# Kernel tuning notes

Hardware: AMD Instinct MI355X
Metric: run time of the kernel (lower is better)

Reference implementation:

```python
import jax, jax.numpy as jnp
import numpy as np

EPS = 1e-5
EMBED_DIM = 1024
CTX_DIM = 768
NUM_HEADS = 16
DH = EMBED_DIM // NUM_HEADS
# Faithful to torch source: embed_dim // num_heads ** 0.5 parses as embed_dim // (num_heads**0.5)
SCALE = EMBED_DIM // (NUM_HEADS ** 0.5)  # = 256.0


def ws_conv1x1(x, w, b, mask):
    # weight-standardized 1x1 conv1d: w [O, I, 1], x [B, I, T]
    w2 = w[..., 0]
    mu = jnp.mean(w2, axis=1, keepdims=True)
    var = jnp.var(w2, axis=1, keepdims=True)
    wn = (w2 - mu) * jax.lax.rsqrt(var + EPS)
    y = jnp.einsum('oi,bit->bot', wn, x) + b[None, :, None]
    if mask is not None:
        y = jnp.where(mask, y, 0.0)  # mask [B,1,T] bool
    return y


def layernorm(x, g, b):
    # normalize over last axis
    mu = jnp.mean(x, axis=-1, keepdims=True)
    var = jnp.var(x, axis=-1, keepdims=True)
    return (x - mu) * jax.lax.rsqrt(var + EPS) * g + b


def setup_inputs() -> dict:
    key = jax.random.key(0)
    ks = jax.random.split(key, 16)
    B, T, S = 4, 1024, 1024
    inp = {
        'x': jax.random.normal(ks[0], (B, EMBED_DIM, T), dtype=jnp.float32),
        'context': jax.random.normal(ks[1], (B, CTX_DIM, S), dtype=jnp.float32),
        'mask': jax.random.randint(ks[2], (B, 1, T), 0, 2).astype(bool),
        'mask_ctx': jax.random.randint(ks[3], (B, 1, S), 0, 2).astype(bool),
        'qw': jax.random.normal(ks[4], (EMBED_DIM, EMBED_DIM, 1), dtype=jnp.float32) * 0.02,
        'qb': jnp.zeros((EMBED_DIM,), jnp.float32),
        'kw': jax.random.normal(ks[5], (EMBED_DIM, CTX_DIM, 1), dtype=jnp.float32) * 0.02,
        'kb': jnp.zeros((EMBED_DIM,), jnp.float32),
        'vw': jax.random.normal(ks[6], (EMBED_DIM, CTX_DIM, 1), dtype=jnp.float32) * 0.02,
        'vb': jnp.zeros((EMBED_DIM,), jnp.float32),
        'ow': jax.random.normal(ks[7], (EMBED_DIM, EMBED_DIM, 1), dtype=jnp.float32) * 0.02,
        'ob': jnp.zeros((EMBED_DIM,), jnp.float32),
        'gq': jnp.ones((DH,), jnp.float32), 'bq': jnp.zeros((DH,), jnp.float32),
        'gk': jnp.ones((DH,), jnp.float32), 'bk': jnp.zeros((DH,), jnp.float32),
        'gv': jnp.ones((DH,), jnp.float32), 'bv': jnp.zeros((DH,), jnp.float32),
    }
    return inp


def reference(x, context, mask, mask_ctx, qw, qb, kw, kb, vw, vb, ow, ob, gq, bq, gk, bk, gv, bv):
    B, E, T = x.shape
    S = context.shape[-1]
    q = ws_conv1x1(x, qw, qb, mask)            # [B,E,T]
    k = ws_conv1x1(context, kw, kb, mask_ctx)  # [B,E,S]
    v = ws_conv1x1(context, vw, vb, mask_ctx)  # [B,E,S]
    # split heads -> [B,H,dh,L]
    q = q.reshape(B, NUM_HEADS, DH, T)
    k = k.reshape(B, NUM_HEADS, DH, S)
    v = v.reshape(B, NUM_HEADS, DH, S)
    # middle_norm: LayerNorm over dh (applied on transposed layout)
    q = jnp.swapaxes(layernorm(jnp.swapaxes(q, -1, -2), gq, bq), -1, -2)
    k = jnp.swapaxes(layernorm(jnp.swapaxes(k, -1, -2), gk, bk), -1, -2)
    v = jnp.swapaxes(layernorm(jnp.swapaxes(v, -1, -2), gv, bv), -1, -2)
    # scores: k^T @ q -> [B,H,S,T]
    scores = jnp.einsum('bhds,bhdt->bhst', k, q) / SCALE
    scores = jnp.where(mask[:, :, None, :], scores, -1e9)  # mask over query dim T
    scores = jax.nn.softmax(scores, axis=-1)               # softmax over T (as in source)
    scores = jnp.where(mask_ctx[:, :, :, None], scores, 0.0)
    out = jnp.einsum('bhds,bhst->bhdt', v, scores)          # v @ scores -> [B,H,dh,T]
    out = out.reshape(B, E, T)
    out = ws_conv1x1(out, ow, ob, mask) + x
    return out
```

## Files before the change

kernel.cpp:

```cpp
#include <hip/hip_runtime.h>

#define NB 4
#define TT 1024
#define SS 1024
#define EE 1024
#define CCH 768
#define NH 16
#define DHH 64
#define EPSF 1e-5f
#define QSCALE (1.4426950408889634f / 256.0f)

typedef unsigned short u16;
typedef __attribute__((ext_vector_type(8))) short short8;
typedef __attribute__((ext_vector_type(8))) unsigned short u16x8;
typedef __attribute__((ext_vector_type(4))) unsigned short u16x4;
typedef __attribute__((ext_vector_type(4))) float f32x4;

__device__ __forceinline__ u16 f2bu(float f) {
    union { float f; unsigned u; } x; x.f = f;
    unsigned r = x.u + 0x7fffu + ((x.u >> 16) & 1u);
    return (u16)(r >> 16);
}
__device__ __forceinline__ float bu2f(u16 u) {
    union { unsigned u; float f; } x; x.u = ((unsigned)u) << 16; return x.f;
}

#if __has_builtin(__builtin_amdgcn_exp2f)
#define EXP2(x) __builtin_amdgcn_exp2f(x)
#else
#define EXP2(x) exp2f(x)
#endif

#define MFMA16(a, b, c) __builtin_amdgcn_mfma_f32_16x16x32_bf16((a), (b), (c), 0, 0, 0)

__device__ __forceinline__ void gload16(const void* g, void* l) {
    __builtin_amdgcn_global_load_lds(
        (const __attribute__((address_space(1))) void*)g,
        (__attribute__((address_space(3))) void*)l, 16, 0, 0);
}

template<int R>
__device__ __forceinline__ void stage_tile(
    const u16* __restrict__ g, int ldg, u16* lds, int w, int lane) {
    constexpr int PW = R / 32;
    int r0 = lane >> 3;
    int cs = ((lane & 7) << 4) ^ (r0 << 4);
#pragma unroll
    for (int j = 0; j < PW; j++) {
        int inst = w * PW + j;
        const u16* src = g + (size_t)(inst * 8 + r0) * ldg + (cs >> 1);
        gload16(src, lds + inst * 512);
    }
}

__device__ __forceinline__ const u16* swz_ptr(const u16* tile, int row, int col) {
    int off = row * 128 + ((col * 2) ^ ((row & 7) << 4));
    return (const u16*)((const char*)tile + off);
}

#define PREP_WS_END   4096
#define PREP_SCAN_END (PREP_WS_END + 8)
#define PREP_TR_END   (PREP_SCAN_END + 1792)
#define PREP_FILL_END (PREP_TR_END + 4096)

__global__ __launch_bounds__(256) void prep(
    const float* __restrict__ qw, const float* __restrict__ kw,
    const float* __restrict__ vw, const float* __restrict__ ow,
    u16* __restrict__ wqn, u16* __restrict__ wkn,
    u16* __restrict__ wvn, u16* __restrict__ won,
    const float* __restrict__ x, const float* __restrict__ ctx,
    const int* __restrict__ mask, const int* __restrict__ mask_ctx,
    u16* __restrict__ xc, u16* __restrict__ cc,
    int* __restrict__ tIdx, int* __restrict__ sIdx,
    int* __restrict__ cntQ, int* __restrict__ cntK,
    float* __restrict__ outF) {
    __shared__ float tile[64][65];
    __shared__ int spos[64], smask[64], wtoti[4];
    __shared__ float sa[4], sb2[4], smean, srstd;
    int bid = blockIdx.x, tid = threadIdx.x;

    if (bid < PREP_WS_END) {
        int mat = bid >> 10, row = bid & 1023;
        const float* w = mat == 0 ? qw : (mat == 1 ? kw : (mat == 2 ? vw : ow));
        u16* wn = mat == 0 ? wqn : (mat == 1 ? wkn : (mat == 2 ? wvn : won));
        int I = (mat == 1 || mat == 2) ? CCH : EE;
        const float* wr = w + (size_t)row * I;
        int nv = I >> 8;
        float vals[4];
        float s = 0.f, s2 = 0.f;
        for (int j = 0; j < nv; j++) {
            float v = wr[tid + 256 * j];
            vals[j] = v; s += v; s2 += v * v;
        }
#pragma unroll
        for (int off = 32; off > 0; off >>= 1) { s += __shfl_down(s, off); s2 += __shfl_down(s2, off); }
        int wid = tid >> 6;
        if ((tid & 63) == 0) { sa[wid] = s; sb2[wid] = s2; }
        __syncthreads();
        if (tid == 0) {
            float ts = sa[0] + sa[1] + sa[2] + sa[3];
            float ts2 = sb2[0] + sb2[1] + sb2[2] + sb2[3];
            float mean = ts / (float)I;
            float var = ts2 / (float)I - mean * mean;
            smean = mean; srstd = rsqrtf(var + EPSF);
        }
        __syncthreads();
        float mean = smean, r = srstd;
        u16* wo = wn + (size_t)row * I;
        for (int j = 0; j < nv; j++) wo[tid + 256 * j] = f2bu((vals[j] - mean) * r);
        return;
    }
    if (bid < PREP_SCAN_END) {
        int t = bid - PREP_WS_END;
        int which = t & 1, b = t >> 1;
        const int* m = (which ? mask_ctx : mask) + b * 1024;
        int* idx = (which ? sIdx : tIdx) + b * 1024;
        int* cnt = (which ? cntK : cntQ) + b;
        int base = tid * 4;
        int v[4]; int s = 0;
#pragma unroll
        for (int i = 0; i < 4; i++) { v[i] = m[base + i] ? 1 : 0; s += v[i]; }
        int lane = tid & 63, wid = tid >> 6;
        int inc = s;
#pragma unroll
        for (int off = 1; off < 64; off <<= 1) {
            int o = __shfl_up(inc, off);
            if (lane >= off) inc += o;
        }
        if (lane == 63) wtoti[wid] = inc;
        __syncthreads();
        int woff = 0;
        for (int i = 0; i < wid; i++) woff += wtoti[i];
        int p = woff + inc - s;
#pragma unroll
        for (int i = 0; i < 4; i++) {
            if (v[i]) idx[p] = base + i;
            p += v[i];
        }
        if (tid == 255) *cnt = p;
        return;
    }
    if (bid < PREP_TR_END) {
        int t = bid - PREP_SCAN_END;
        int xb = t & 15; int rem = t >> 4;
        int yy = rem % 28, b = rem / 28;
        int mat = yy < 16 ? 0 : 1;
        int r0 = (mat == 0 ? yy : yy - 16) * 64;
        int R = mat == 0 ? EE : CCH;
        const float* in = mat == 0 ? x : ctx;
        const int* m = (mat == 0 ? mask : mask_ctx) + (size_t)b * 1024;
        u16* out = mat == 0 ? xc : cc;
        int c0 = xb * 64;
        const float* ip = in + (size_t)b * R * 1024;
        u16* op = out + (size_t)b * R * 1024;
#pragma unroll
        for (int mm = 0; mm < 16; mm++) {
            int id = tid + 256 * mm; int r = id >> 6, c = id & 63;
            tile[r][c] = ip[(size_t)(r0 + r) * 1024 + c0 + c];
        }
        int base = tid * 4;
        int v[4]; int s = 0;
#pragma unroll
        for (int i = 0; i < 4; i++) { v[i] = m[base + i] ? 1 : 0; s += v[i]; }
        int lane = tid & 63, wid = tid >> 6;
        int inc = s;
#pragma unroll
        for (int off = 1; off < 64; off <<= 1) {
            int o = __shfl_up(inc, off);
            if (lane >= off) inc += o;
        }
        if (lane == 63) wtoti[wid] = inc;
        __syncthreads();
        int woff = 0;
        for (int i = 0; i < wid; i++) woff += wtoti[i];
        int p = woff + inc - s;
#pragma unroll
        for (int i = 0; i < 4; i++) {
            int g = base + i;
            if (g >= c0 && g < c0 + 64) { spos[g - c0] = p; smask[g - c0] = v[i]; }
            p += v[i];
        }
        __syncthreads();
#pragma unroll
        for (int mm = 0; mm < 16; mm++) {
            int id = tid + 256 * mm; int rr = id >> 6, cc2 = id & 63;
            if (smask[rr])
                op[(size_t)spos[rr] * R + r0 + cc2] = f2bu(tile[cc2][rr]);
        }
        return;
    }
    {
        int f = bid - PREP_TR_END;
        int b = f >> 10, o = f & 1023;
        const float* xr = x + ((size_t)b * EE + o) * TT;
        float* orow = outF + ((size_t)b * EE + o) * TT;
        const int* mrow = mask + (size_t)b * TT;
        int4 mv = ((const int4*)mrow)[tid];
        float4 xv = ((const float4*)xr)[tid];
        int t4 = tid * 4;
        if (!mv.x) orow[t4 + 0] = xv.x;
        if (!mv.y) orow[t4 + 1] = xv.y;
        if (!mv.z) orow[t4 + 2] = xv.z;
        if (!mv.w) orow[t4 + 3] = xv.w;
    }
}

__device__ __forceinline__ void gemm_core(
    const u16* __restrict__ A, const u16* __restrict__ Bp, int I,
    int o0, int l0, u16 (*at)[128][64], u16 (*bt)[64][64], f32x4 (&acc)[4][2]) {
    int tid = threadIdx.x;
    int w = tid >> 6, lane = tid & 63, quad = lane >> 4, l16 = lane & 15;
    int wm = w & 1, wn = w >> 1;
    const u16* Ab = A + (size_t)o0 * I;
    const u16* Bb = Bp + (size_t)l0 * I;
    stage_tile<128>(Ab, I, &at[0][0][0], w, lane);
    stage_tile<64>(Bb, I, &bt[0][0][0], w, lane);
    __syncthreads();
    int cur = 0;
    for (int k0 = 0; k0 < I; k0 += 64, cur ^= 1) {
        int kn = k0 + 64;
        if (kn < I) {
            stage_tile<128>(Ab + kn, I, &at[cur ^ 1][0][0], w, lane);
            stage_tile<64>(Bb + kn, I, &bt[cur ^ 1][0][0], w, lane);
        }
#pragma unroll
        for (int ks = 0; ks < 64; ks += 32) {
            short8 af[4], bf[2];
#pragma unroll
            for (int i = 0; i < 4; i++)
                af[i] = *(const short8*)swz_ptr(&at[cur][0][0], wm * 64 + i * 16 + l16, ks + quad * 8);
#pragma unroll
            for (int j = 0; j < 2; j++)
                bf[j] = *(const short8*)swz_ptr(&bt[cur][0][0], wn * 32 + j * 16 + l16, ks + quad * 8);
#pragma unroll
            for (int mt = 0; mt < 4; mt++)
#pragma unroll
                for (int nt = 0; nt < 2; nt++)
                    acc[mt][nt] = MFMA16(af[mt], bf[nt], acc[mt][nt]);
        }
        __syncthreads();
    }
}

__global__ __launch_bounds__(256) void proj_qkv(
    const u16* __restrict__ wq, const u16* __restrict__ wk, const u16* __restrict__ wv,
    const u16* __restrict__ xc, const u16* __restrict__ cc,
    const float* __restrict__ qb, const float* __restrict__ kb, const float* __restrict__ vbi,
    const int* __restrict__ cntQ, const int* __restrict__ cntK,
    const float* __restrict__ gq, const float* __restrict__ bq,
    const float* __restrict__ gk, const float* __restrict__ bk,
    const float* __restrict__ gv, const float* __restrict__ bv,
    u16* __restrict__ qc, u16* __restrict__ kc, u16* __restrict__ vn) {
    int mat = blockIdx.x >> 3;
    int o0 = (blockIdx.x & 7) * 128;
    int l0 = blockIdx.y * 64;
    int b = blockIdx.z;
    int limit = (mat == 0) ? cntQ[b] : cntK[b];
    if (l0 >= limit) return;
    __shared__ u16 at[2][128][64];
    __shared__ u16 bt[2][64][64];
    __shared__ float sg[64], sbe[64], sbias[128];
    int tid = threadIdx.x;
    int w = tid >> 6, lane = tid & 63, quad = lane >> 4, l16 = lane & 15;
    int wm = w & 1, wn = w >> 1;
    const u16* A = mat == 0 ? wq : (mat == 1 ? wk : wv);
    const u16* BT = mat == 0 ? xc : cc;
    const float* bias = mat == 0 ? qb : (mat == 1 ? kb : vbi);
    int I = mat == 0 ? EE : CCH;
    if (tid < 64) {
        const float* gsrc = mat == 0 ? gq : (mat == 1 ? gk : gv);
        const float* bsrc = mat == 0 ? bq : (mat == 1 ? bk : bv);
        sg[tid] = gsrc[tid];
        sbe[tid] = bsrc[tid];
    }
    if (tid < 128) sbias[tid] = bias[o0 + tid];

    f32x4 acc[4][2] = {};
    gemm_core(A, BT + (size_t)b * 1024 * I, I, o0, l0, at, bt, acc);

    float scale = mat == 0 ? QSCALE : 1.0f;
    int h = (o0 >> 6) + wm;
    int bh = b * NH + h;
#pragma unroll
    for (int nt = 0; nt < 2; nt++) {
        int l = l0 + wn * 32 + nt * 16 + l16;
        float vbuf[16];
        float s = 0.f;
#pragma unroll
        for (int mt = 0; mt < 4; mt++)
#pragma unroll
            for (int reg = 0; reg < 4; reg++) {
                float v = acc[mt][nt][reg] + sbias[wm * 64 + mt * 16 + quad * 4 + reg];
                vbuf[mt * 4 + reg] = v; s += v;
            }
        s += __shfl_xor(s, 16); s += __shfl_xor(s, 32);
        float mean = s * (1.f / 64);
        float s2 = 0.f;
#pragma unroll
        for (int i = 0; i < 16; i++) { float dv = vbuf[i] - mean; s2 += dv * dv; }
        s2 += __shfl_xor(s2, 16); s2 += __shfl_xor(s2, 32);
        float r = rsqrtf(s2 * (1.f / 64) + EPSF);
        if (l < limit) {
            if (mat < 2) {
                u16* outT = mat == 0 ? qc : kc;
                u16* op = outT + ((size_t)bh * 1024 + l) * 64;
#pragma unroll
                for (int mt = 0; mt < 4; mt++) {
                    u16x4 pk;
#pragma unroll
                    for (int reg = 0; reg < 4; reg++) {
                        int d = mt * 16 + quad * 4 + reg;
                        pk[reg] = f2bu(((vbuf[mt * 4 + reg] - mean) * r * sg[d] + sbe[d]) * scale);
                    }
                    *(u16x4*)&op[mt * 16 + quad * 4] = pk;
                }
            } else {
#pragma unroll
                for (int mt = 0; mt < 4; mt++)
#pragma unroll
                    for (int reg = 0; reg < 4; reg++) {
                        int d = mt * 16 + quad * 4 + reg;
                        vn[((size_t)b * EE + h * 64 + d) * 1024 + l] =
                            f2bu((vbuf[mt * 4 + reg] - mean) * r * sg[d] + sbe[d]);
                    }
            }
        }
    }
}

__global__ __launch_bounds__(256) void attn_stats_mfma(
    const u16* __restrict__ qc, const u16* __restrict__ kc,
    const int* __restrict__ cntQ, const int* __restrict__ cntK,
    u16* __restrict__ vn, u16* __restrict__ P) {
    int s0 = blockIdx.x * 64, h = blockIdx.y, b = blockIdx.z;
    int Sc = cntK[b], Tc = cntQ[b];
    if (s0 >= Sc) return;
    __shared__ u16 kt[64][64];
    __shared__ u16 qt[2][64][64];
    __shared__ float lp[4][64];
    int tid = threadIdx.x;
    int w = tid >> 6, lane = tid & 63, quad = lane >> 4, l16 = lane & 15;
    int head = b * NH + h;
    const u16* kp = kc + (size_t)head * SS * DHH;
    const u16* qp = qc + (size_t)head * TT * DHH;
    u16* Pb = P + (size_t)head * TT * SS;
    stage_tile<64>(kp + (size_t)s0 * DHH, DHH, &kt[0][0], w, lane);
    stage_tile<64>(qp, DHH, &qt[0][0][0], w, lane);
    __syncthreads();
    float rl[4][4] = {};
    int cur = 0;
    for (int t0 = 0; t0 < Tc; t0 += 64, cur ^= 1) {
        if (t0 + 64 < Tc)
            stage_tile<64>(qp + (size_t)(t0 + 64) * DHH, DHH, &qt[cur ^ 1][0][0], w, lane);
        f32x4 acc[4] = {};
#pragma unroll
        for (int ks = 0; ks < 64; ks += 32) {
            short8 bf = *(const short8*)swz_ptr(&qt[cur][0][0], w * 16 + l16, ks + quad * 8);
#pragma unroll
            for (int mt = 0; mt < 4; mt++) {
                short8 af = *(const short8*)swz_ptr(&kt[0][0], mt * 16 + l16, ks + quad * 8);
                acc[mt] = MFMA16(af, bf, acc[mt]);
            }
        }
        int tcol = t0 + w * 16 + l16;
        int tok = tcol < Tc;
#pragma unroll
        for (int mt = 0; mt < 4; mt++) {
            u16x4 pk;
#pragma unroll
            for (int reg = 0; reg < 4; reg++) {
                int sl = s0 + mt * 16 + quad * 4 + reg;
                float e = EXP2(acc[mt][reg]);
                if (tok) rl[mt][reg] += e;
                pk[reg] = (sl < Sc) ? f2bu(e) : (u16)0;
            }
            *(u16x4*)&Pb[(size_t)tcol * SS + s0 + mt * 16 + quad * 4] = pk;
        }
        __syncthreads();
    }
#pragma unroll
    for (int mt = 0; mt < 4; mt++) {
#pragma unroll
        for (int reg = 0; reg < 4; reg++) {
            float v = rl[mt][reg];
            v += __shfl_xor(v, 1); v += __shfl_xor(v, 2);
            v += __shfl_xor(v, 4); v += __shfl_xor(v, 8);
            if (l16 == 0) lp[w][mt * 16 + quad * 4 + reg] = v;
        }
    }
    __syncthreads();
    {
        int so = tid & 63, dg = tid >> 6;
        int s = s0 + so;
        float lv = lp[0][so] + lp[1][so] + lp[2][so] + lp[3][so];
        float wsc = (lv > 0.f) ? (1.f / lv) : 0.f;
        u16* vrow = vn + ((size_t)b * EE + h * 64) * SS;
        int live = s < Sc;
#pragma unroll
        for (int i = 0; i < 16; i++) {
            int d = dg * 16 + i;
            size_t a = (size_t)d * SS + s;
            vrow[a] = live ? f2bu(bu2f(vrow[a]) * wsc) : (u16)0;
        }
    }
}

__global__ __launch_bounds__(256) void attn_pv_mfma(
    const u16* __restrict__ vn, const u16* __restrict__ P,
    const int* __restrict__ cntQ, const int* __restrict__ cntK,
    u16* __restrict__ ac) {
    int t0 = blockIdx.x * 64, h = blockIdx.y, b = blockIdx.z;
    int Tc = cntQ[b], Sc = cntK[b];
    if (t0 >= Tc) return;
    int Kc = (Sc + 63) & ~63;
    __shared__ u16 at[2][64][64];
    __shared__ u16 bt[2][64][64];
    __shared__ u16 pt[64][72];
    int tid = threadIdx.x;
    int w = tid >> 6, lane = tid & 63, quad = lane >> 4, l16 = lane & 15;
    int head = b * NH + h;
    const u16* vp = vn + ((size_t)head * DHH) * SS;
    const u16* Pb = P + (size_t)head * TT * SS + (size_t)t0 * SS;
    f32x4 oacc[4] = {};
    if (Kc > 0) {
        stage_tile<64>(vp, SS, &at[0][0][0], w, lane);
        stage_tile<64>(Pb, SS, &bt[0][0][0], w, lane);
        __syncthreads();
        int cur = 0;
        for (int k0 = 0; k0 < Kc; k0 += 64, cur ^= 1) {
            int kn = k0 + 64;
            if (kn < Kc) {
                stage_tile<64>(vp + kn, SS, &at[cur ^ 1][0][0], w, lane);
                stage_tile<64>(Pb + kn, SS, &bt[cur ^ 1][0][0], w, lane);
            }
#pragma unroll
            for (int ks = 0; ks < 64; ks += 32) {
                short8 bf = *(const short8*)swz_ptr(&bt[cur][0][0], w * 16 + l16, ks + quad * 8);
#pragma unroll
                for (int mt = 0; mt < 4; mt++) {
                    short8 af = *(const short8*)swz_ptr(&at[cur][0][0], mt * 16 + l16, ks + quad * 8);
                    oacc[mt] = MFMA16(af, bf, oacc[mt]);
                }
            }
            __syncthreads();
        }
    }
    int tl = w * 16 + l16;
#pragma unroll
    for (int mt = 0; mt < 4; mt++) {
        u16x4 pk;
#pragma unroll
        for (int reg = 0; reg < 4; reg++) pk[reg] = f2bu(oacc[mt][reg]);
        *(u16x4*)&pt[tl][mt * 16 + quad * 4] = pk;
    }
    __syncthreads();
#pragma unroll
    for (int i = 0; i < 2; i++) {
        int id = tid * 2 + i;
        int r = id >> 3, c = (id & 7) * 8;
        if (t0 + r < Tc)
            *(u16x8*)&ac[((size_t)b * TT + t0 + r) * EE + h * 64 + c] =
                *(const u16x8*)&pt[r][c];
    }
}

__global__ __launch_bounds__(256) void proj_o(
    const u16* __restrict__ won, const u16* __restrict__ ac,
    const float* __restrict__ obi, const int* __restrict__ tIdx,
    const int* __restrict__ cntQ, const float* __restrict__ x,
    float* __restrict__ out) {
    int o0 = blockIdx.x * 128, l0 = blockIdx.y * 64, b = blockIdx.z;
    int Tc = cntQ[b];
    if (l0 >= Tc) return;
    __shared__ u16 at[2][128][64];
    __shared__ u16 bt[2][64][64];
    __shared__ float sbias[128];
    __shared__ int stre[64];
    int tid = threadIdx.x;
    int w = tid >> 6, lane = tid & 63, quad = lane >> 4, l16 = lane & 15;
    int wm = w & 1, wn = w >> 1;
    if (tid < 128) sbias[tid] = obi[o0 + tid];
    if (tid < 64) stre[tid] = tIdx[(size_t)b * 1024 + l0 + tid];
    f32x4 acc[4][2] = {};
    gemm_core(won, ac + (size_t)b * TT * EE, EE, o0, l0, at, bt, acc);
#pragma unroll
    for (int nt = 0; nt < 2; nt++) {
        int lcol = wn * 32 + nt * 16 + l16;
        int l = l0 + lcol;
        if (l < Tc) {
            int treal = stre[lcol];
#pragma unroll
            for (int mt = 0; mt < 4; mt++)
#pragma unroll
                for (int reg = 0; reg < 4; reg++) {
                    int o = o0 + wm * 64 + mt * 16 + quad * 4 + reg;
                    size_t off = ((size_t)b * EE + o) * TT + treal;
                    out[off] = acc[mt][nt][reg] + sbias[wm * 64 + mt * 16 + quad * 4 + reg] + x[off];
                }
        }
    }
}

extern "C" void kernel_launch(void* const* d_in, const int* in_sizes, int n_in,
                              void* d_out, int out_size, void* d_ws, size_t ws_size,
                              hipStream_t stream) {
    const float* x        = (const float*)d_in[0];
    const float* ctx      = (const float*)d_in[1];
    const int*   mask     = (const int*)d_in[2];
    const int*   mask_ctx = (const int*)d_in[3];
    const float* qw  = (const float*)d_in[4];
    const float* qbi = (const float*)d_in[5];
    const float* kw  = (const float*)d_in[6];
    const float* kbi = (const float*)d_in[7];
    const float* vw  = (const float*)d_in[8];
    const float* vbi = (const float*)d_in[9];
    const float* ow  = (const float*)d_in[10];
    const float* obi = (const float*)d_in[11];
    const float* gq = (const float*)d_in[12];
    const float* bq = (const float*)d_in[13];
    const float* gk = (const float*)d_in[14];
    const float* bk = (const float*)d_in[15];
    const float* gv = (const float*)d_in[16];
    const float* bv = (const float*)d_in[17];

    u16* p = (u16*)d_ws;
    u16* wqn = p; p += (size_t)EE * EE;
    u16* wkn = p; p += (size_t)EE * CCH;
    u16* wvn = p; p += (size_t)EE * CCH;
    u16* won = p; p += (size_t)EE * EE;
    u16* xc  = p; p += (size_t)NB * TT * EE;
    u16* cc  = p; p += (size_t)NB * SS * CCH;
    u16* vn  = p; p += (size_t)NB * EE * SS;
    u16* qc  = p; p += (size_t)NB * NH * TT * DHH;
    u16* kc  = p; p += (size_t)NB * NH * SS * DHH;
    u16* ac  = p; p += (size_t)NB * TT * EE;
    u16* P   = p; p += (size_t)NB * NH * TT * SS;
    int* tIdx = (int*)p;
    int* sIdx = tIdx + NB * 1024;
    int* cntQ = sIdx + NB * 1024;
    int* cntK = cntQ + NB;

    prep<<<PREP_FILL_END, 256, 0, stream>>>(
        qw, kw, vw, ow, wqn, wkn, wvn, won, x, ctx, mask, mask_ctx,
        xc, cc, tIdx, sIdx, cntQ, cntK, (float*)d_out);

    proj_qkv<<<dim3(24, 16, NB), 256, 0, stream>>>(
        wqn, wkn, wvn, xc, cc, qbi, kbi, vbi, cntQ, cntK,
        gq, bq, gk, bk, gv, bv, qc, kc, vn);

    attn_stats_mfma<<<dim3(16, NH, NB), 256, 0, stream>>>(
        qc, kc, cntQ, cntK, vn, P);

    attn_pv_mfma<<<dim3(16, NH, NB), 256, 0, stream>>>(
        vn, P, cntQ, cntK, ac);

    proj_o<<<dim3(8, 16, NB), 256, 0, stream>>>(
        won, ac, obi, tIdx, cntQ, x, (float*)d_out);
}
```

Measured before the change: 227.1 us.

## Fuse all stages into one persistent kernel with software grid barriers

Merges the five separate kernel launches (prep, QKV projection, attention stats, PV, output projection) into a single persistent kernel of 512 blocks. Each block loops over the former blocks of every stage, and atomic-counter grid barriers sit between stages. Shared memory becomes a union of the per-stage layouts. This removes launch gaps and tail effects between kernels, but it assumes all 512 blocks are co-resident and adds spin-wait barrier cost, along with possible occupancy limits from the union-sized LDS and the launch bound of two blocks per CU.

```diff
diff --git a/kernel.cpp b/kernel.cpp
--- a/kernel.cpp
+++ b/kernel.cpp
@@ -10,6 +10,8 @@
 #define EPSF 1e-5f
 #define QSCALE (1.4426950408889634f / 256.0f)
 
+#define GRID_BLKS 512
+
 typedef unsigned short u16;
 typedef __attribute__((ext_vector_type(8))) short short8;
 typedef __attribute__((ext_vector_type(8))) unsigned short u16x8;
@@ -32,6 +34,21 @@
 #endif
 
 #define MFMA16(a, b, c) __builtin_amdgcn_mfma_f32_16x16x32_bf16((a), (b), (c), 0, 0, 0)
+
+__device__ unsigned int g_cnt[8];
+
+__device__ __forceinline__ void grid_barrier(int idx) {
+    __syncthreads();
+    if (threadIdx.x == 0) {
+        __threadfence();
+        unsigned ticket = atomicAdd(&g_cnt[idx], 1u);
+        unsigned target = (ticket / GRID_BLKS + 1u) * GRID_BLKS;
+        while (atomicAdd(&g_cnt[idx], 0u) < target)
+            __builtin_amdgcn_s_sleep(2);
+        __threadfence();
+    }
+    __syncthreads();
+}
 
 __device__ __forceinline__ void gload16(const void* g, void* l) {
     __builtin_amdgcn_global_load_lds(
@@ -63,26 +80,54 @@
 #define PREP_TR_END   (PREP_SCAN_END + 1792)
 #define PREP_FILL_END (PREP_TR_END + 4096)
 
-__global__ __launch_bounds__(256) void prep(
-    const float* __restrict__ qw, const float* __restrict__ kw,
-    const float* __restrict__ vw, const float* __restrict__ ow,
-    u16* __restrict__ wqn, u16* __restrict__ wkn,
-    u16* __restrict__ wvn, u16* __restrict__ won,
-    const float* __restrict__ x, const float* __restrict__ ctx,
-    const int* __restrict__ mask, const int* __restrict__ mask_ctx,
-    u16* __restrict__ xc, u16* __restrict__ cc,
-    int* __restrict__ tIdx, int* __restrict__ sIdx,
-    int* __restrict__ cntQ, int* __restrict__ cntK,
-    float* __restrict__ outF) {
-    __shared__ float tile[64][65];
-    __shared__ int spos[64], smask[64], wtoti[4];
-    __shared__ float sa[4], sb2[4], smean, srstd;
-    int bid = blockIdx.x, tid = threadIdx.x;
-
+union SMem {
+    struct {
+        float tile[64][65];
+        int spos[64], smask[64], wtoti[4];
+        float sa[4], sb2[4], smean, srstd;
+    } pr;
+    struct {
+        u16 at[2][128][64];
+        u16 bt[2][64][64];
+        float sg[64], sbe[64], sbias[128];
+    } qk;
+    struct {
+        u16 kt[64][64];
+        u16 qt[2][64][64];
+        float lp[4][64];
+    } st;
+    struct {
+        u16 at[2][64][64];
+        u16 bt[2][64][64];
+        u16 pt[64][72];
+    } pv;
+    struct {
+        u16 at[2][128][64];
+        u16 bt[2][64][64];
+        float sbias[128];
+        int stre[64];
+    } po;
+};
+
+struct KArgs {
+    const float *qw, *kw, *vw, *ow;
+    u16 *wqn, *wkn, *wvn, *won;
+    const float *x, *ctx;
+    const int *mask, *mask_ctx;
+    u16 *xc, *cc;
+    int *tIdx, *sIdx, *cntQ, *cntK;
+    float *outF;
+    const float *qb, *kb, *vbi, *obi;
+    const float *gq, *bq, *gk, *bk, *gv, *bv;
+    u16 *qc, *kc, *vn, *ac, *P;
+};
+
+__device__ void prep_body(int bid, const KArgs& a, SMem& sm) {
+    int tid = threadIdx.x;
     if (bid < PREP_WS_END) {
         int mat = bid >> 10, row = bid & 1023;
-        const float* w = mat == 0 ? qw : (mat == 1 ? kw : (mat == 2 ? vw : ow));
-        u16* wn = mat == 0 ? wqn : (mat == 1 ? wkn : (mat == 2 ? wvn : won));
+        const float* w = mat == 0 ? a.qw : (mat == 1 ? a.kw : (mat == 2 ? a.vw : a.ow));
+        u16* wn = mat == 0 ? a.wqn : (mat == 1 ? a.wkn : (mat == 2 ? a.wvn : a.won));
         int I = (mat == 1 || mat == 2) ? CCH : EE;
         const float* wr = w + (size_t)row * I;
         int nv = I >> 8;
@@ -95,17 +140,17 @@
 #pragma unroll
         for (int off = 32; off > 0; off >>= 1) { s += __shfl_down(s, off); s2 += __shfl_down(s2, off); }
         int wid = tid >> 6;
-        if ((tid & 63) == 0) { sa[wid] = s; sb2[wid] = s2; }
+        if ((tid & 63) == 0) { sm.pr.sa[wid] = s; sm.pr.sb2[wid] = s2; }
         __syncthreads();
         if (tid == 0) {
-            float ts = sa[0] + sa[1] + sa[2] + sa[3];
-            float ts2 = sb2[0] + sb2[1] + sb2[2] + sb2[3];
+            float ts = sm.pr.sa[0] + sm.pr.sa[1] + sm.pr.sa[2] + sm.pr.sa[3];
+            float ts2 = sm.pr.sb2[0] + sm.pr.sb2[1] + sm.pr.sb2[2] + sm.pr.sb2[3];
             float mean = ts / (float)I;
             float var = ts2 / (float)I - mean * mean;
-            smean = mean; srstd = rsqrtf(var + EPSF);
-        }
-        __syncthreads();
-        float mean = smean, r = srstd;
+            sm.pr.smean = mean; sm.pr.srstd = rsqrtf(var + EPSF);
+        }
+        __syncthreads();
+        float mean = sm.pr.smean, r = sm.pr.srstd;
         u16* wo = wn + (size_t)row * I;
         for (int j = 0; j < nv; j++) wo[tid + 256 * j] = f2bu((vals[j] - mean) * r);
         return;
@@ -113,9 +158,9 @@
     if (bid < PREP_SCAN_END) {
         int t = bid - PREP_WS_END;
         int which = t & 1, b = t >> 1;
-        const int* m = (which ? mask_ctx : mask) + b * 1024;
-        int* idx = (which ? sIdx : tIdx) + b * 1024;
-        int* cnt = (which ? cntK : cntQ) + b;
+        const int* m = (which ? a.mask_ctx : a.mask) + b * 1024;
+        int* idx = (which ? a.sIdx : a.tIdx) + b * 1024;
+        int* cnt = (which ? a.cntK : a.cntQ) + b;
         int base = tid * 4;
         int v[4]; int s = 0;
 #pragma unroll
@@ -127,10 +172,10 @@
             int o = __shfl_up(inc, off);
             if (lane >= off) inc += o;
         }
-        if (lane == 63) wtoti[wid] = inc;
+        if (lane == 63) sm.pr.wtoti[wid] = inc;
         __syncthreads();
         int woff = 0;
-        for (int i = 0; i < wid; i++) woff += wtoti[i];
+        for (int i = 0; i < wid; i++) woff += sm.pr.wtoti[i];
         int p = woff + inc - s;
 #pragma unroll
         for (int i = 0; i < 4; i++) {
@@ -147,16 +192,16 @@
         int mat = yy < 16 ? 0 : 1;
         int r0 = (mat == 0 ? yy : yy - 16) * 64;
         int R = mat == 0 ? EE : CCH;
-        const float* in = mat == 0 ? x : ctx;
-        const int* m = (mat == 0 ? mask : mask_ctx) + (size_t)b * 1024;
-        u16* out = mat == 0 ? xc : cc;
+        const float* in = mat == 0 ? a.x : a.ctx;
+        const int* m = (mat == 0 ? a.mask : a.mask_ctx) + (size_t)b * 1024;
+        u16* out = mat == 0 ? a.xc : a.cc;
         int c0 = xb * 64;
         const float* ip = in + (size_t)b * R * 1024;
         u16* op = out + (size_t)b * R * 1024;
 #pragma unroll
         for (int mm = 0; mm < 16; mm++) {
             int id = tid + 256 * mm; int r = id >> 6, c = id & 63;
-            tile[r][c] = ip[(size_t)(r0 + r) * 1024 + c0 + c];
+            sm.pr.tile[r][c] = ip[(size_t)(r0 + r) * 1024 + c0 + c];
         }
         int base = tid * 4;
         int v[4]; int s = 0;
@@ -169,32 +214,32 @@
             int o = __shfl_up(inc, off);
             if (lane >= off) inc += o;
         }
-        if (lane == 63) wtoti[wid] = inc;
+        if (lane == 63) sm.pr.wtoti[wid] = inc;
         __syncthreads();
         int woff = 0;
-        for (int i = 0; i < wid; i++) woff += wtoti[i];
+        for (int i = 0; i < wid; i++) woff += sm.pr.wtoti[i];
         int p = woff + inc - s;
 #pragma unroll
         for (int i = 0; i < 4; i++) {
             int g = base + i;
-            if (g >= c0 && g < c0 + 64) { spos[g - c0] = p; smask[g - c0] = v[i]; }
+            if (g >= c0 && g < c0 + 64) { sm.pr.spos[g - c0] = p; sm.pr.smask[g - c0] = v[i]; }
             p += v[i];
         }
         __syncthreads();
 #pragma unroll
         for (int mm = 0; mm < 16; mm++) {
             int id = tid + 256 * mm; int rr = id >> 6, cc2 = id & 63;
-            if (smask[rr])
-                op[(size_t)spos[rr] * R + r0 + cc2] = f2bu(tile[cc2][rr]);
+            if (sm.pr.smask[rr])
+                op[(size_t)sm.pr.spos[rr] * R + r0 + cc2] = f2bu(sm.pr.tile[cc2][rr]);
         }
         return;
     }
     {
         int f = bid - PREP_TR_END;
         int b = f >> 10, o = f & 1023;
-        const float* xr = x + ((size_t)b * EE + o) * TT;
-        float* orow = outF + ((size_t)b * EE + o) * TT;
-        const int* mrow = mask + (size_t)b * TT;
+        const float* xr = a.x + ((size_t)b * EE + o) * TT;
+        float* orow = a.outF + ((size_t)b * EE + o) * TT;
+        const int* mrow = a.mask + (size_t)b * TT;
         int4 mv = ((const int4*)mrow)[tid];
         float4 xv = ((const float4*)xr)[tid];
         int t4 = tid * 4;
@@ -242,41 +287,31 @@
     }
 }
 
-__global__ __launch_bounds__(256) void proj_qkv(
-    const u16* __restrict__ wq, const u16* __restrict__ wk, const u16* __restrict__ wv,
-    const u16* __restrict__ xc, const u16* __restrict__ cc,
-    const float* __restrict__ qb, const float* __restrict__ kb, const float* __restrict__ vbi,
-    const int* __restrict__ cntQ, const int* __restrict__ cntK,
-    const float* __restrict__ gq, const float* __restrict__ bq,
-    const float* __restrict__ gk, const float* __restrict__ bk,
-    const float* __restrict__ gv, const float* __restrict__ bv,
-    u16* __restrict__ qc, u16* __restrict__ kc, u16* __restrict__ vn) {
-    int mat = blockIdx.x >> 3;
-    int o0 = (blockIdx.x & 7) * 128;
-    int l0 = blockIdx.y * 64;
-    int b = blockIdx.z;
-    int limit = (mat == 0) ? cntQ[b] : cntK[b];
+__device__ void qkv_body(int vb, const KArgs& a, SMem& sm) {
+    int gx = vb % 24, rem = vb / 24;
+    int gy = rem & 15, b = rem >> 4;
+    int mat = gx >> 3;
+    int o0 = (gx & 7) * 128;
+    int l0 = gy * 64;
+    int limit = (mat == 0) ? a.cntQ[b] : a.cntK[b];
     if (l0 >= limit) return;
-    __shared__ u16 at[2][128][64];
-    __shared__ u16 bt[2][64][64];
-    __shared__ float sg[64], sbe[64], sbias[128];
     int tid = threadIdx.x;
     int w = tid >> 6, lane = tid & 63, quad = lane >> 4, l16 = lane & 15;
     int wm = w & 1, wn = w >> 1;
-    const u16* A = mat == 0 ? wq : (mat == 1 ? wk : wv);
-    const u16* BT = mat == 0 ? xc : cc;
-    const float* bias = mat == 0 ? qb : (mat == 1 ? kb : vbi);
+    const u16* A = mat == 0 ? a.wqn : (mat == 1 ? a.wkn : a.wvn);
+    const u16* BT = mat == 0 ? a.xc : a.cc;
+    const float* bias = mat == 0 ? a.qb : (mat == 1 ? a.kb : a.vbi);
     int I = mat == 0 ? EE : CCH;
     if (tid < 64) {
-        const float* gsrc = mat == 0 ? gq : (mat == 1 ? gk : gv);
-        const float* bsrc = mat == 0 ? bq : (mat == 1 ? bk : bv);
-        sg[tid] = gsrc[tid];
-        sbe[tid] = bsrc[tid];
-    }
-    if (tid < 128) sbias[tid] = bias[o0 + tid];
+        const float* gsrc = mat == 0 ? a.gq : (mat == 1 ? a.gk : a.gv);
+        const float* bsrc = mat == 0 ? a.bq : (mat == 1 ? a.bk : a.bv);
+        sm.qk.sg[tid] = gsrc[tid];
+        sm.qk.sbe[tid] = bsrc[tid];
+    }
+    if (tid < 128) sm.qk.sbias[tid] = bias[o0 + tid];
 
     f32x4 acc[4][2] = {};
-    gemm_core(A, BT + (size_t)b * 1024 * I, I, o0, l0, at, bt, acc);
+    gemm_core(A, BT + (size_t)b * 1024 * I, I, o0, l0, sm.qk.at, sm.qk.bt, acc);
 
     float scale = mat == 0 ? QSCALE : 1.0f;
     int h = (o0 >> 6) + wm;
@@ -290,7 +325,7 @@
         for (int mt = 0; mt < 4; mt++)
 #pragma unroll
             for (int reg = 0; reg < 4; reg++) {
-                float v = acc[mt][nt][reg] + sbias[wm * 64 + mt * 16 + quad * 4 + reg];
+                float v = acc[mt][nt][reg] + sm.qk.sbias[wm * 64 + mt * 16 + quad * 4 + reg];
                 vbuf[mt * 4 + reg] = v; s += v;
             }
         s += __shfl_xor(s, 16); s += __shfl_xor(s, 32);
@@ -302,7 +337,7 @@
         float r = rsqrtf(s2 * (1.f / 64) + EPSF);
         if (l < limit) {
             if (mat < 2) {
-                u16* outT = mat == 0 ? qc : kc;
+                u16* outT = mat == 0 ? a.qc : a.kc;
                 u16* op = outT + ((size_t)bh * 1024 + l) * 64;
 #pragma unroll
                 for (int mt = 0; mt < 4; mt++) {
@@ -310,7 +345,7 @@
 #pragma unroll
                     for (int reg = 0; reg < 4; reg++) {
                         int d = mt * 16 + quad * 4 + reg;
-                        pk[reg] = f2bu(((vbuf[mt * 4 + reg] - mean) * r * sg[d] + sbe[d]) * scale);
+                        pk[reg] = f2bu(((vbuf[mt * 4 + reg] - mean) * r * sm.qk.sg[d] + sm.qk.sbe[d]) * scale);
                     }
                     *(u16x4*)&op[mt * 16 + quad * 4] = pk;
                 }
@@ -320,45 +355,41 @@
 #pragma unroll
                     for (int reg = 0; reg < 4; reg++) {
                         int d = mt * 16 + quad * 4 + reg;
-                        vn[((size_t)b * EE + h * 64 + d) * 1024 + l] =
-                            f2bu((vbuf[mt * 4 + reg] - mean) * r * sg[d] + sbe[d]);
+                        a.vn[((size_t)b * EE + h * 64 + d) * 1024 + l] =
+                            f2bu((vbuf[mt * 4 + reg] - mean) * r * sm.qk.sg[d] + sm.qk.sbe[d]);
                     }
             }
         }
     }
 }
 
-__global__ __launch_bounds__(256) void attn_stats_mfma(
-    const u16* __restrict__ qc, const u16* __restrict__ kc,
-    const int* __restrict__ cntQ, const int* __restrict__ cntK,
-    u16* __restrict__ vn, u16* __restrict__ P) {
-    int s0 = blockIdx.x * 64, h = blockIdx.y, b = blockIdx.z;
-    int Sc = cntK[b], Tc = cntQ[b];
+__device__ void stats_body(int vb, const KArgs& a, SMem& sm) {
+    int gx = vb & 15, rem = vb >> 4;
+    int h = rem & 15, b = rem >> 4;
+    int s0 = gx * 64;
+    int Sc = a.cntK[b], Tc = a.cntQ[b];
     if (s0 >= Sc) return;
-    __shared__ u16 kt[64][64];
-    __shared__ u16 qt[2][64][64];
-    __shared__ float lp[4][64];
     int tid = threadIdx.x;
     int w = tid >> 6, lane = tid & 63, quad = lane >> 4, l16 = lane & 15;
     int head = b * NH + h;
-    const u16* kp = kc + (size_t)head * SS * DHH;
-    const u16* qp = qc + (size_t)head * TT * DHH;
-    u16* Pb = P + (size_t)head * TT * SS;
-    stage_tile<64>(kp + (size_t)s0 * DHH, DHH, &kt[0][0], w, lane);
-    stage_tile<64>(qp, DHH, &qt[0][0][0], w, lane);
+    const u16* kp = a.kc + (size_t)head * SS * DHH;
+    const u16* qp = a.qc + (size_t)head * TT * DHH;
+    u16* Pb = a.P + (size_t)head * TT * SS;
+    stage_tile<64>(kp + (size_t)s0 * DHH, DHH, &sm.st.kt[0][0], w, lane);
+    stage_tile<64>(qp, DHH, &sm.st.qt[0][0][0], w, lane);
     __syncthreads();
     float rl[4][4] = {};
     int cur = 0;
     for (int t0 = 0; t0 < Tc; t0 += 64, cur ^= 1) {
         if (t0 + 64 < Tc)
-            stage_tile<64>(qp + (size_t)(t0 + 64) * DHH, DHH, &qt[cur ^ 1][0][0], w, lane);
+            stage_tile<64>(qp + (size_t)(t0 + 64) * DHH, DHH, &sm.st.qt[cur ^ 1][0][0], w, lane);
         f32x4 acc[4] = {};
 #pragma unroll
         for (int ks = 0; ks < 64; ks += 32) {
-            short8 bf = *(const short8*)swz_ptr(&qt[cur][0][0], w * 16 + l16, ks + quad * 8);
+            short8 bf = *(const short8*)swz_ptr(&sm.st.qt[cur][0][0], w * 16 + l16, ks + quad * 8);
 #pragma unroll
             for (int mt = 0; mt < 4; mt++) {
-                short8 af = *(const short8*)swz_ptr(&kt[0][0], mt * 16 + l16, ks + quad * 8);
+                short8 af = *(const short8*)swz_ptr(&sm.st.kt[0][0], mt * 16 + l16, ks + quad * 8);
                 acc[mt] = MFMA16(af, bf, acc[mt]);
             }
         }
@@ -385,60 +416,56 @@
             float v = rl[mt][reg];
             v += __shfl_xor(v, 1); v += __shfl_xor(v, 2);
             v += __shfl_xor(v, 4); v += __shfl_xor(v, 8);
-            if (l16 == 0) lp[w][mt * 16 + quad * 4 + reg] = v;
+            if (l16 == 0) sm.st.lp[w][mt * 16 + quad * 4 + reg] = v;
         }
     }
     __syncthreads();
     {
         int so = tid & 63, dg = tid >> 6;
         int s = s0 + so;
-        float lv = lp[0][so] + lp[1][so] + lp[2][so] + lp[3][so];
+        float lv = sm.st.lp[0][so] + sm.st.lp[1][so] + sm.st.lp[2][so] + sm.st.lp[3][so];
         float wsc = (lv > 0.f) ? (1.f / lv) : 0.f;
-        u16* vrow = vn + ((size_t)b * EE + h * 64) * SS;
+        u16* vrow = a.vn + ((size_t)b * EE + h * 64) * SS;
         int live = s < Sc;
 #pragma unroll
         for (int i = 0; i < 16; i++) {
             int d = dg * 16 + i;
-            size_t a = (size_t)d * SS + s;
-            vrow[a] = live ? f2bu(bu2f(vrow[a]) * wsc) : (u16)0;
-        }
-    }
-}
-
-__global__ __launch_bounds__(256) void attn_pv_mfma(
-    const u16* __restrict__ vn, const u16* __restrict__ P,
-    const int* __restrict__ cntQ, const int* __restrict__ cntK,
-    u16* __restrict__ ac) {
-    int t0 = blockIdx.x * 64, h = blockIdx.y, b = blockIdx.z;
-    int Tc = cntQ[b], Sc = cntK[b];
+            size_t ad = (size_t)d * SS + s;
+            vrow[ad] = live ? f2bu(bu2f(vrow[ad]) * wsc) : (u16)0;
+        }
+    }
+}
+
+__device__ void pv_body(int vb, const KArgs& a, SMem& sm) {
+    int gx = vb & 15, rem = vb >> 4;
+    int h = rem & 15, b = rem >> 4;
+    int t0 = gx * 64;
+    int Tc = a.cntQ[b], Sc = a.cntK[b];
     if (t0 >= Tc) return;
     int Kc = (Sc + 63) & ~63;
-    __shared__ u16 at[2][64][64];
-    __shared__ u16 bt[2][64][64];
-    __shared__ u16 pt[64][72];
     int tid = threadIdx.x;
     int w = tid >> 6, lane = tid & 63, quad = lane >> 4, l16 = lane & 15;
     int head = b * NH + h;
-    const u16* vp = vn + ((size_t)head * DHH) * SS;
-    const u16* Pb = P + (size_t)head * TT * SS + (size_t)t0 * SS;
+    const u16* vp = a.vn + ((size_t)head * DHH) * SS;
+    const u16* Pb = a.P + (size_t)head * TT * SS + (size_t)t0 * SS;
     f32x4 oacc[4] = {};
     if (Kc > 0) {
-        stage_tile<64>(vp, SS, &at[0][0][0], w, lane);
-        stage_tile<64>(Pb, SS, &bt[0][0][0], w, lane);
+        stage_tile<64>(vp, SS, &sm.pv.at[0][0][0], w, lane);
+        stage_tile<64>(Pb, SS, &sm.pv.bt[0][0][0], w, lane);
         __syncthreads();
         int cur = 0;
         for (int k0 = 0; k0 < Kc; k0 += 64, cur ^= 1) {
             int kn = k0 + 64;
             if (kn < Kc) {
-                stage_tile<64>(vp + kn, SS, &at[cur ^ 1][0][0], w, lane);
-                stage_tile<64>(Pb + kn, SS, &bt[cur ^ 1][0][0], w, lane);
+                stage_tile<64>(vp + kn, SS, &sm.pv.at[cur ^ 1][0][0], w, lane);
+                stage_tile<64>(Pb + kn, SS, &sm.pv.bt[cur ^ 1][0][0], w, lane);
             }
 #pragma unroll
             for (int ks = 0; ks < 64; ks += 32) {
-                short8 bf = *(const short8*)swz_ptr(&bt[cur][0][0], w * 16 + l16, ks + quad * 8);
+                short8 bf = *(const short8*)swz_ptr(&sm.pv.bt[cur][0][0], w * 16 + l16, ks + quad * 8);
 #pragma unroll
                 for (int mt = 0; mt < 4; mt++) {
-                    short8 af = *(const short8*)swz_ptr(&at[cur][0][0], mt * 16 + l16, ks + quad * 8);
+                    short8 af = *(const short8*)swz_ptr(&sm.pv.at[cur][0][0], mt * 16 + l16, ks + quad * 8);
                     oacc[mt] = MFMA16(af, bf, oacc[mt]);
                 }
             }
@@ -451,7 +478,7 @@
         u16x4 pk;
 #pragma unroll
         for (int reg = 0; reg < 4; reg++) pk[reg] = f2bu(oacc[mt][reg]);
-        *(u16x4*)&pt[tl][mt * 16 + quad * 4] = pk;
+        *(u16x4*)&sm.pv.pt[tl][mt * 16 + quad * 4] = pk;
     }
     __syncthreads();
 #pragma unroll
@@ -459,101 +486,112 @@
         int id = tid * 2 + i;
         int r = id >> 3, c = (id & 7) * 8;
         if (t0 + r < Tc)
-            *(u16x8*)&ac[((size_t)b * TT + t0 + r) * EE + h * 64 + c] =
-                *(const u16x8*)&pt[r][c];
-    }
-}
-
-__global__ __launch_bounds__(256) void proj_o(
-    const u16* __restrict__ won, const u16* __restrict__ ac,
-    const float* __restrict__ obi, const int* __restrict__ tIdx,
-    const int* __restrict__ cntQ, const float* __restrict__ x,
-    float* __restrict__ out) {
-    int o0 = blockIdx.x * 128, l0 = blockIdx.y * 64, b = blockIdx.z;
-    int Tc = cntQ[b];
+            *(u16x8*)&a.ac[((size_t)b * TT + t0 + r) * EE + h * 64 + c] =
+                *(const u16x8*)&sm.pv.pt[r][c];
+    }
+}
+
+__device__ void po_body(int vb, const KArgs& a, SMem& sm) {
+    int gx = vb & 7, rem = vb >> 3;
+    int gy = rem & 15, b = rem >> 4;
+    int o0 = gx * 128, l0 = gy * 64;
+    int Tc = a.cntQ[b];
     if (l0 >= Tc) return;
-    __shared__ u16 at[2][128][64];
-    __shared__ u16 bt[2][64][64];
-    __shared__ float sbias[128];
-    __shared__ int stre[64];
     int tid = threadIdx.x;
     int w = tid >> 6, lane = tid & 63, quad = lane >> 4, l16 = lane & 15;
     int wm = w & 1, wn = w >> 1;
-    if (tid < 128) sbias[tid] = obi[o0 + tid];
-    if (tid < 64) stre[tid] = tIdx[(size_t)b * 1024 + l0 + tid];
+    if (tid < 128) sm.po.sbias[tid] = a.obi[o0 + tid];
+    if (tid < 64) sm.po.stre[tid] = a.tIdx[(size_t)b * 1024 + l0 + tid];
     f32x4 acc[4][2] = {};
-    gemm_core(won, ac + (size_t)b * TT * EE, EE, o0, l0, at, bt, acc);
+    gemm_core(a.won, a.ac + (size_t)b * TT * EE, EE, o0, l0, sm.po.at, sm.po.bt, acc);
 #pragma unroll
     for (int nt = 0; nt < 2; nt++) {
         int lcol = wn * 32 + nt * 16 + l16;
         int l = l0 + lcol;
         if (l < Tc) {
-            int treal = stre[lcol];
+            int treal = sm.po.stre[lcol];
 #pragma unroll
             for (int mt = 0; mt < 4; mt++)
 #pragma unroll
                 for (int reg = 0; reg < 4; reg++) {
                     int o = o0 + wm * 64 + mt * 16 + quad * 4 + reg;
                     size_t off = ((size_t)b * EE + o) * TT + treal;
-                    out[off] = acc[mt][nt][reg] + sbias[wm * 64 + mt * 16 + quad * 4 + reg] + x[off];
+                    a.outF[off] = acc[mt][nt][reg] + sm.po.sbias[wm * 64 + mt * 16 + quad * 4 + reg] + a.x[off];
                 }
         }
+    }
+}
+
+__global__ __launch_bounds__(256, 2) void mega(KArgs a) {
+    __shared__ SMem sm;
+    int bid0 = blockIdx.x;
+
+    for (int vb = bid0; vb < PREP_FILL_END; vb += GRID_BLKS) {
+        prep_body(vb, a, sm);
+        __syncthreads();
+    }
+    grid_barrier(0);
+    for (int vb = bid0; vb < 24 * 16 * NB; vb += GRID_BLKS) {
+        qkv_body(vb, a, sm);
+        __syncthreads();
+    }
+    grid_barrier(1);
+    for (int vb = bid0; vb < 16 * NH * NB; vb += GRID_BLKS) {
+        stats_body(vb, a, sm);
+        __syncthreads();
+    }
+    grid_barrier(2);
+    for (int vb = bid0; vb < 16 * NH * NB; vb += GRID_BLKS) {
+        pv_body(vb, a, sm);
+        __syncthreads();
+    }
+    grid_barrier(3);
+    for (int vb = bid0; vb < 8 * 16 * NB; vb += GRID_BLKS) {
+        po_body(vb, a, sm);
+        __syncthreads();
     }
 }
 
 extern "C" void kernel_launch(void* const* d_in, const int* in_sizes, int n_in,
                               void* d_out, int out_size, void* d_ws, size_t ws_size,
                               hipStream_t stream) {
-    const float* x        = (const float*)d_in[0];
-    const float* ctx      = (const float*)d_in[1];
-    const int*   mask     = (const int*)d_in[2];
-    const int*   mask_ctx = (const int*)d_in[3];
-    const float* qw  = (const float*)d_in[4];
-    const float* qbi = (const float*)d_in[5];
-    const float* kw  = (const float*)d_in[6];
-    const float* kbi = (const float*)d_in[7];
-    const float* vw  = (const float*)d_in[8];
-    const float* vbi = (const float*)d_in[9];
-    const float* ow  = (const float*)d_in[10];
-    const float* obi = (const float*)d_in[11];
-    const float* gq = (const float*)d_in[12];
-    const float* bq = (const float*)d_in[13];
-    const float* gk = (const float*)d_in[14];
-    const float* bk = (const float*)d_in[15];
-    const float* gv = (const float*)d_in[16];
-    const float* bv = (const float*)d_in[17];
+    KArgs a;
+    a.x        = (const float*)d_in[0];
+    a.ctx      = (const float*)d_in[1];
+    a.mask     = (const int*)d_in[2];
+    a.mask_ctx = (const int*)d_in[3];
+    a.qw  = (const float*)d_in[4];
+    a.qb  = (const float*)d_in[5];
+    a.kw  = (const float*)d_in[6];
+    a.kb  = (const float*)d_in[7];
+    a.vw  = (const float*)d_in[8];
+    a.vbi = (const float*)d_in[9];
+    a.ow  = (const float*)d_in[10];
+    a.obi = (const float*)d_in[11];
+    a.gq = (const float*)d_in[12];
+    a.bq = (const float*)d_in[13];
+    a.gk = (const float*)d_in[14];
+    a.bk = (const float*)d_in[15];
+    a.gv = (const float*)d_in[16];
+    a.bv = (const float*)d_in[17];
 
     u16* p = (u16*)d_ws;
-    u16* wqn = p; p += (size_t)EE * EE;
-    u16* wkn = p; p += (size_t)EE * CCH;
-    u16* wvn = p; p += (size_t)EE * CCH;
-    u16* won = p; p += (size_t)EE * EE;
-    u16* xc  = p; p += (size_t)NB * TT * EE;
-    u16* cc  = p; p += (size_t)NB * SS * CCH;
-    u16* vn  = p; p += (size_t)NB * EE * SS;
-    u16* qc  = p; p += (size_t)NB * NH * TT * DHH;
-    u16* kc  = p; p += (size_t)NB * NH * SS * DHH;
-    u16* ac  = p; p += (size_t)NB * TT * EE;
-    u16* P   = p; p += (size_t)NB * NH * TT * SS;
-    int* tIdx = (int*)p;
-    int* sIdx = tIdx + NB * 1024;
-    int* cntQ = sIdx + NB * 1024;
-    int* cntK = cntQ + NB;
-
-    prep<<<PREP_FILL_END, 256, 0, stream>>>(
-        qw, kw, vw, ow, wqn, wkn, wvn, won, x, ctx, mask, mask_ctx,
-        xc, cc, tIdx, sIdx, cntQ, cntK, (float*)d_out);
-
-    proj_qkv<<<dim3(24, 16, NB), 256, 0, stream>>>(
-        wqn, wkn, wvn, xc, cc, qbi, kbi, vbi, cntQ, cntK,
-        gq, bq, gk, bk, gv, bv, qc, kc, vn);
-
-    attn_stats_mfma<<<dim3(16, NH, NB), 256, 0, stream>>>(
-        qc, kc, cntQ, cntK, vn, P);
-
-    attn_pv_mfma<<<dim3(16, NH, NB), 256, 0, stream>>>(
-        vn, P, cntQ, cntK, ac);
-
-    proj_o<<<dim3(8, 16, NB), 256, 0, stream>>>(
-        won, ac, obi, tIdx, cntQ, x, (float*)d_out);
-}
+    a.wqn = p; p += (size_t)EE * EE;
+    a.wkn = p; p += (size_t)EE * CCH;
+    a.wvn = p; p += (size_t)EE * CCH;
+    a.won = p; p += (size_t)EE * EE;
+    a.xc  = p; p += (size_t)NB * TT * EE;
+    a.cc  = p; p += (size_t)NB * SS * CCH;
+    a.vn  = p; p += (size_t)NB * EE * SS;
+    a.qc  = p; p += (size_t)NB * NH * TT * DHH;
+    a.kc  = p; p += (size_t)NB * NH * SS * DHH;
+    a.ac  = p; p += (size_t)NB * TT * EE;
+    a.P   = p; p += (size_t)NB * NH * TT * SS;
+    a.tIdx = (int*)p;
+    a.sIdx = a.tIdx + NB * 1024;
+    a.cntQ = a.sIdx + NB * 1024;
+    a.cntK = a.cntQ + NB;
+    a.outF = (float*)d_out;
+
+    mega<<<dim3(GRID_BLKS), dim3(256), 0, stream>>>(a);
+}
```

Result: slower. 518.8 us (+128.4%).
